# Performance work log

Hardware: AMD Instinct MI355X
Metric: run time of the kernel (lower is better)

## Reference

```python
import jax, jax.numpy as jnp
import numpy as np

E = 1024
H = 16
D = E // H  # head_dim = 64


def setup_inputs() -> dict:
    key = jax.random.key(0)
    k_x, k_w1, k_b1, k_w2, k_b2 = jax.random.split(key, 5)
    s = 1.0 / np.sqrt(E)
    return {
        "x": jax.random.normal(k_x, (2, 2048, E), dtype=jnp.float32),
        "qkv_w": jax.random.uniform(k_w1, (3 * E, E), jnp.float32, -s, s),
        "qkv_b": jax.random.uniform(k_b1, (3 * E,), jnp.float32, -s, s),
        "out_w": jax.random.uniform(k_w2, (E, E), jnp.float32, -s, s),
        "out_b": jax.random.uniform(k_b2, (E,), jnp.float32, -s, s),
    }


def reference(x, qkv_w, qkv_b, out_w, out_b):
    B, T, _ = x.shape
    # qkv projection (torch Linear: x @ W.T + b)
    qkv = x @ qkv_w.T + qkv_b  # [B, T, 3E]
    q, k, v = jnp.split(qkv, 3, axis=-1)
    # [B, T, E] -> [B, H, T, D]
    def to_heads(t):
        return t.reshape(B, T, H, D).transpose(0, 2, 1, 3)
    q, k, v = to_heads(q), to_heads(k), to_heads(v)
    scale = 1.0 / np.sqrt(D).astype(np.float32)
    scores = jnp.einsum("bhqd,bhkd->bhqk", q, k) * scale  # [B, H, T, T]
    attn = jax.nn.softmax(scores, axis=-1)
    # dropout is identity in eval mode
    out = jnp.einsum("bhqk,bhkd->bhqd", attn, v)  # [B, H, T, D]
    out = out.transpose(0, 2, 1, 3).reshape(B, T, E)
    return out @ out_w.T + out_b
```

## Files before the change

### kernel.cpp

```cpp
#include <hip/hip_runtime.h>

#define TT 2048
#define BB 2
#define EE 1024
#define HH 16
#define DD 64
#define E3 3072
#define NTOK 4096

typedef unsigned short u16;
typedef _Float16 __attribute__((ext_vector_type(8))) half8;
typedef __fp16 __attribute__((ext_vector_type(2))) fp16x2;
typedef __attribute__((ext_vector_type(4))) float f32x4;

__device__ __forceinline__ unsigned f2h(float f) {
    union { _Float16 h; u16 u; } v; v.h = (_Float16)f; return (unsigned)v.u;
}
__device__ __forceinline__ unsigned pkh(float a, float b) {
    union { fp16x2 h; unsigned u; } v;
    v.h = __builtin_amdgcn_cvt_pkrtz(a, b);
    return v.u;
}

__device__ __forceinline__ void async_ld16(const u16* g, const u16* l) {
    auto gp = reinterpret_cast<const __attribute__((address_space(1))) unsigned*>(
        reinterpret_cast<uintptr_t>(g));
    auto lp = reinterpret_cast<__attribute__((address_space(3))) unsigned*>(
        reinterpret_cast<uintptr_t>(l));
    __builtin_amdgcn_global_load_lds(gp, lp, 16, 0, 0);
}

__global__ __launch_bounds__(256) void split3(
    const float* __restrict__ x, const float* __restrict__ w1,
    const float* __restrict__ w2,
    u16* __restrict__ xh, u16* __restrict__ w1h, u16* __restrict__ w2h)
{
    const int N1 = (NTOK * EE) / 4;
    const int N2 = N1 + (E3 * EE) / 4;
    int i = blockIdx.x * 256 + threadIdx.x;
    const float* src; u16* dst; int j;
    if (i < N1)      { src = x;  dst = xh;  j = i; }
    else if (i < N2) { src = w1; dst = w1h; j = i - N1; }
    else             { src = w2; dst = w2h; j = i - N2; }
    float4 v = ((const float4*)src)[j];
    *(uint2*)&dst[(size_t)j * 4] = make_uint2(
        f2h(v.x) | (f2h(v.y) << 16), f2h(v.z) | (f2h(v.w) << 16));
}

template <int WMT, bool QSCALE, bool F16OUT>
__global__ __launch_bounds__(256, 3) void gemm_f16(
    const u16* __restrict__ Ag, const u16* __restrict__ Wg,
    const float* __restrict__ bias, void* __restrict__ Cout,
    u16* __restrict__ vtp, int M, int N)
{
    constexpr int BM = WMT * 32;
    constexpr int APASS = BM / 32;
    __shared__ u16 sAB[(BM + 128) * 64];
    u16* sA = sAB;
    u16* sB = sAB + BM * 64;

    const int tid  = threadIdx.x;
    const int lane = tid & 63;
    const int wave = tid >> 6;
    const int quad = lane >> 4;
    const int l16  = lane & 15;
    const int wm = wave >> 1, wn = wave & 1;
    const int m0 = blockIdx.y * BM;
    const int n0 = blockIdx.x * 128;

    const int srow = tid >> 3;
    const int schk = tid & 7;

    const u16* ag[APASS]; int aldw[APASS];
#pragma unroll
    for (int p = 0; p < APASS; ++p) {
        int row = p * 32 + srow;
        ag[p] = Ag + (size_t)(m0 + row) * EE + ((schk ^ (row & 7)) << 3);
        aldw[p] = (p * 256 + wave * 64) * 8;
    }
    const u16* bg[4]; int bldw[4];
#pragma unroll
    for (int p = 0; p < 4; ++p) {
        int row = p * 32 + srow;
        bg[p] = Wg + (size_t)(n0 + row) * EE + ((schk ^ (row & 7)) << 3);
        bldw[p] = (p * 256 + wave * 64) * 8;
    }

    f32x4 acc[WMT][4];
#pragma unroll
    for (int mt = 0; mt < WMT; ++mt)
#pragma unroll
        for (int nt = 0; nt < 4; ++nt) acc[mt][nt] = (f32x4){0.f, 0.f, 0.f, 0.f};

    for (int k0 = 0; k0 < EE; k0 += 64) {
        __syncthreads();
#pragma unroll
        for (int p = 0; p < APASS; ++p) async_ld16(ag[p] + k0, sA + aldw[p]);
#pragma unroll
        for (int p = 0; p < 4; ++p)    async_ld16(bg[p] + k0, sB + bldw[p]);
        __syncthreads();

        half8 fa[WMT][2], fb[4][2];
#pragma unroll
        for (int mt = 0; mt < WMT; ++mt) {
            int r = wm * (WMT * 16) + mt * 16 + l16;
#pragma unroll
            for (int ks = 0; ks < 2; ++ks)
                fa[mt][ks] = *(const half8*)&sA[r * 64 + (((ks * 4 + quad) ^ (r & 7)) << 3)];
        }
#pragma unroll
        for (int nt = 0; nt < 4; ++nt) {
            int r = wn * 64 + nt * 16 + l16;
#pragma unroll
            for (int ks = 0; ks < 2; ++ks)
                fb[nt][ks] = *(const half8*)&sB[r * 64 + (((ks * 4 + quad) ^ (r & 7)) << 3)];
        }
#pragma unroll
        for (int ks = 0; ks < 2; ++ks)
#pragma unroll
            for (int mt = 0; mt < WMT; ++mt)
#pragma unroll
                for (int nt = 0; nt < 4; ++nt)
                    acc[mt][nt] = __builtin_amdgcn_mfma_f32_16x16x32_f16(
                        fa[mt][ks], fb[nt][ks], acc[mt][nt], 0, 0, 0);
    }

    const float scale = (QSCALE && n0 < EE) ? 0.18033688011112042f : 1.0f;
    float bv[4];
#pragma unroll
    for (int nt = 0; nt < 4; ++nt) bv[nt] = bias[n0 + wn * 64 + nt * 16 + l16];

    if constexpr (F16OUT) {
        if (vtp != nullptr && n0 >= 2 * EE) {
            __syncthreads();
            u16* tile = sAB;
#pragma unroll
            for (int mt = 0; mt < WMT; ++mt)
#pragma unroll
                for (int nt = 0; nt < 4; ++nt) {
                    int c  = wn * 64 + nt * 16 + l16;
                    int ub = (wm * 16 + mt * 4 + quad) ^ ((c & 7) << 1);
                    *(uint2*)&tile[c * 128 + ub * 4] = make_uint2(
                        f2h(acc[mt][nt][0] + bv[nt]) | (f2h(acc[mt][nt][1] + bv[nt]) << 16),
                        f2h(acc[mt][nt][2] + bv[nt]) | (f2h(acc[mt][nt][3] + bv[nt]) << 16));
                }
            __syncthreads();
            const int c    = tid >> 1;
            const int hf   = tid & 1;
            const int hd   = ((n0 - 2 * EE) >> 6) + (c >> 6);
            const int d    = c & 63;
            const int bq   = m0 >> 11;
            u16* dst = vtp + ((size_t)(bq * HH + hd) * DD + d) * TT
                           + (m0 & (TT - 1)) + hf * 64;
#pragma unroll
            for (int j = 0; j < 8; ++j) {
                int u = (hf * 16 + j * 2) ^ ((c & 7) << 1);
                *(uint4*)(dst + j * 8) = *(const uint4*)&tile[c * 128 + u * 4];
            }
            return;
        }
    }

#pragma unroll
    for (int mt = 0; mt < WMT; ++mt)
#pragma unroll
        for (int nt = 0; nt < 4; ++nt)
#pragma unroll
            for (int r = 0; r < 4; ++r) {
                int rg = m0 + wm * (WMT * 16) + mt * 16 + quad * 4 + r;
                int cg = n0 + wn * 64 + nt * 16 + l16;
                float v = (acc[mt][nt][r] + bv[nt]) * scale;
                if (F16OUT) ((u16*)Cout)[(size_t)rg * N + cg] = (u16)f2h(v);
                else        ((float*)Cout)[(size_t)rg * N + cg] = v;
            }
}

__global__ __launch_bounds__(256, 4) void attn_mfma(
    const u16* __restrict__ qkv, const u16* __restrict__ vt,
    u16* __restrict__ obuf)
{
    __shared__ u16 KB[2][64][64];
    __shared__ u16 VB[2][64][64];
    __shared__ u16 PB[4][16][64];

    const int tid  = threadIdx.x;
    const int wave = tid >> 6;
    const int lane = tid & 63;
    const int quad = lane >> 4;
    const int l16  = lane & 15;

    const int q0 = blockIdx.x * 64;
    const int hh = blockIdx.y;
    const int b  = blockIdx.z;

    const int srow = tid >> 3;
    const int schk = tid & 7;
    const int ldsw = wave * 512;

    half8 qb[2];
    {
        int row = q0 + wave * 16 + l16;
        const u16* qg = qkv + (size_t)(b * TT + row) * E3 + hh * DD;
        qb[0] = *(const half8*)(qg + quad * 8);
        qb[1] = *(const half8*)(qg + 32 + quad * 8);
    }

#pragma unroll
    for (int p = 0; p < 2; ++p) {
        int row = p * 32 + srow;
        int sw8 = (schk ^ (row & 7)) << 3;
        async_ld16(qkv + (size_t)(b * TT + row) * E3 + EE + hh * DD + sw8,
                   &KB[0][0][0] + p * 2048 + ldsw);
        async_ld16(vt + ((size_t)(b * HH + hh) * DD + row) * TT + sw8,
                   &VB[0][0][0] + p * 2048 + ldsw);
    }
    __syncthreads();

    const f32x4 Z = {0.f, 0.f, 0.f, 0.f};
    float l_i = 0.f;
    f32x4 o[4];
#pragma unroll
    for (int dt = 0; dt < 4; ++dt) o[dt] = (f32x4){0.f, 0.f, 0.f, 0.f};

    const int px = (l16 & 7) << 1;
    u16* prow = &PB[wave][l16][0];

    int cur = 0;
    for (int kt = 0; kt < TT; kt += 64, cur ^= 1) {
        const int ktn = (kt + 64) & (TT - 1);
#pragma unroll
        for (int p = 0; p < 2; ++p) {
            int row = p * 32 + srow;
            int sw8 = (schk ^ (row & 7)) << 3;
            async_ld16(qkv + (size_t)(b * TT + ktn + row) * E3 + EE + hh * DD + sw8,
                       &KB[cur ^ 1][0][0] + p * 2048 + ldsw);
            async_ld16(vt + ((size_t)(b * HH + hh) * DD + row) * TT + ktn + sw8,
                       &VB[cur ^ 1][0][0] + p * 2048 + ldsw);
        }

#pragma unroll
        for (int kg = 0; kg < 4; ++kg) {
            int r0 = kg * 16 + l16;
            half8 kf0 = *(const half8*)&KB[cur][r0][((quad)     ^ (r0 & 7)) << 3];
            half8 kf1 = *(const half8*)&KB[cur][r0][((4 + quad) ^ (r0 & 7)) << 3];
            f32x4 t = __builtin_amdgcn_mfma_f32_16x16x32_f16(kf0, qb[0], Z, 0, 0, 0);
            f32x4 s = __builtin_amdgcn_mfma_f32_16x16x32_f16(kf1, qb[1], t, 0, 0, 0);
            float p0 = __builtin_amdgcn_exp2f(s[0]);
            float p1 = __builtin_amdgcn_exp2f(s[1]);
            float p2 = __builtin_amdgcn_exp2f(s[2]);
            float p3 = __builtin_amdgcn_exp2f(s[3]);
            l_i += (p0 + p1) + (p2 + p3);
            int pu = (kg * 4 + quad) ^ px;
            *(uint2*)&prow[pu * 4] = make_uint2(pkh(p0, p1), pkh(p2, p3));
        }

#pragma unroll
        for (int kb = 0; kb < 2; ++kb) {
            half8 pf = *(const half8*)&prow[((kb * 8 + quad * 2) ^ px) << 2];
#pragma unroll
            for (int dt = 0; dt < 4; ++dt) {
                int vr = dt * 16 + l16;
                half8 vf = *(const half8*)&VB[cur][vr][((kb * 4 + quad) ^ (vr & 7)) << 3];
                o[dt] = __builtin_amdgcn_mfma_f32_16x16x32_f16(vf, pf, o[dt], 0, 0, 0);
            }
        }

        __syncthreads();
    }

    float inv;
    {
        float l = l_i;
        l += __shfl_xor(l, 16, 64);
        l += __shfl_xor(l, 32, 64);
        inv = 1.f / l;
    }
    {
        size_t base = (size_t)(b * TT + q0 + wave * 16 + l16) * EE + hh * DD;
#pragma unroll
        for (int dt = 0; dt < 4; ++dt) {
            unsigned h0 = f2h(o[dt][0] * inv), h1 = f2h(o[dt][1] * inv);
            unsigned h2 = f2h(o[dt][2] * inv), h3 = f2h(o[dt][3] * inv);
            *(uint2*)&obuf[base + dt * 16 + quad * 4] =
                make_uint2(h0 | (h1 << 16), h2 | (h3 << 16));
        }
    }
}

extern "C" void kernel_launch(void* const* d_in, const int* in_sizes, int n_in,
                              void* d_out, int out_size, void* d_ws, size_t ws_size,
                              hipStream_t stream)
{
    const float* x     = (const float*)d_in[0];
    const float* qkv_w = (const float*)d_in[1];
    const float* qkv_b = (const float*)d_in[2];
    const float* out_w = (const float*)d_in[3];
    const float* out_b = (const float*)d_in[4];
    float* out = (float*)d_out;

    const size_t NX  = (size_t)NTOK * EE;
    const size_t NW1 = (size_t)E3 * EE;
    const size_t NW2 = (size_t)EE * EE;
    const size_t NQ  = (size_t)NTOK * E3;

    u16* ws   = (u16*)d_ws;
    u16* x_h  = ws;
    u16* w1h  = ws + NX;
    u16* w2h  = w1h + NW1;
    u16* qkvb = w2h + NW2;
    u16* vtb  = qkvb + NQ;

    split3<<<dim3((unsigned)((NX + NW1 + NW2) / 4 / 256)), 256, 0, stream>>>(
        x, qkv_w, out_w, x_h, w1h, w2h);

    gemm_f16<4, true, true><<<dim3(E3 / 128, NTOK / 128), 256, 0, stream>>>(
        x_h, w1h, qkv_b, (void*)qkvb, vtb, NTOK, E3);

    attn_mfma<<<dim3(TT / 64, HH, BB), 256, 0, stream>>>(qkvb, vtb, x_h);

    gemm_f16<2, false, false><<<dim3(EE / 128, NTOK / 64), 256, 0, stream>>>(
        x_h, w2h, out_b, (void*)out, nullptr, NTOK, EE);
}
```

Baseline: 183.9 us.

## Restructure attention around 32x32 MFMA with register-resident probabilities

```diff
diff --git a/kernel.cpp b/kernel.cpp
--- a/kernel.cpp
+++ b/kernel.cpp
@@ -12,6 +12,7 @@
 typedef _Float16 __attribute__((ext_vector_type(8))) half8;
 typedef __fp16 __attribute__((ext_vector_type(2))) fp16x2;
 typedef __attribute__((ext_vector_type(4))) float f32x4;
+typedef __attribute__((ext_vector_type(16))) float f32x16;
 
 __device__ __forceinline__ unsigned f2h(float f) {
     union { _Float16 h; u16 u; } v; v.h = (_Float16)f; return (unsigned)v.u;
@@ -175,115 +176,125 @@
             }
 }
 
-__global__ __launch_bounds__(256, 4) void attn_mfma(
+__global__ __launch_bounds__(256, 2) void attn_mfma(
     const u16* __restrict__ qkv, const u16* __restrict__ vt,
     u16* __restrict__ obuf)
 {
-    __shared__ u16 KB[2][64][64];
-    __shared__ u16 VB[2][64][64];
-    __shared__ u16 PB[4][16][64];
+    __shared__ u16 VB[2][64][128];
 
     const int tid  = threadIdx.x;
     const int wave = tid >> 6;
     const int lane = tid & 63;
-    const int quad = lane >> 4;
-    const int l16  = lane & 15;
-
-    const int q0 = blockIdx.x * 64;
+    const int l31  = lane & 31;
+    const int h    = lane >> 5;
+
+    const int q0 = blockIdx.x * 128;
     const int hh = blockIdx.y;
     const int b  = blockIdx.z;
 
-    const int srow = tid >> 3;
-    const int schk = tid & 7;
-    const int ldsw = wave * 512;
-
-    half8 qb[2];
+    const int vrw  = lane >> 4;
+    const int vchk = lane & 15;
+
+    const u16* vbase = vt + (size_t)(b * HH + hh) * DD * TT;
+
+#pragma unroll
+    for (int p = 0; p < 4; ++p) {
+        int row = wave * 16 + p * 4 + vrw;
+        async_ld16(vbase + (size_t)row * TT + ((vchk ^ (row & 7)) << 3),
+                   &VB[0][0][0] + (wave * 16 + p * 4) * 128);
+    }
+
+    half8 qb[4];
     {
-        int row = q0 + wave * 16 + l16;
-        const u16* qg = qkv + (size_t)(b * TT + row) * E3 + hh * DD;
-        qb[0] = *(const half8*)(qg + quad * 8);
-        qb[1] = *(const half8*)(qg + 32 + quad * 8);
-    }
-
-#pragma unroll
-    for (int p = 0; p < 2; ++p) {
-        int row = p * 32 + srow;
-        int sw8 = (schk ^ (row & 7)) << 3;
-        async_ld16(qkv + (size_t)(b * TT + row) * E3 + EE + hh * DD + sw8,
-                   &KB[0][0][0] + p * 2048 + ldsw);
-        async_ld16(vt + ((size_t)(b * HH + hh) * DD + row) * TT + sw8,
-                   &VB[0][0][0] + p * 2048 + ldsw);
+        const u16* qg = qkv + (size_t)(b * TT + q0 + wave * 32 + l31) * E3 + hh * DD;
+#pragma unroll
+        for (int ks = 0; ks < 4; ++ks)
+            qb[ks] = *(const half8*)(qg + ks * 16 + h * 8);
     }
     __syncthreads();
 
-    const f32x4 Z = {0.f, 0.f, 0.f, 0.f};
+    f32x16 o[2];
+#pragma unroll
+    for (int dt = 0; dt < 2; ++dt)
+#pragma unroll
+        for (int j = 0; j < 16; ++j) o[dt][j] = 0.f;
     float l_i = 0.f;
-    f32x4 o[4];
-#pragma unroll
-    for (int dt = 0; dt < 4; ++dt) o[dt] = (f32x4){0.f, 0.f, 0.f, 0.f};
-
-    const int px = (l16 & 7) << 1;
-    u16* prow = &PB[wave][l16][0];
+
+    const f32x16 Z16 = {};
 
     int cur = 0;
-    for (int kt = 0; kt < TT; kt += 64, cur ^= 1) {
-        const int ktn = (kt + 64) & (TT - 1);
-#pragma unroll
-        for (int p = 0; p < 2; ++p) {
-            int row = p * 32 + srow;
-            int sw8 = (schk ^ (row & 7)) << 3;
-            async_ld16(qkv + (size_t)(b * TT + ktn + row) * E3 + EE + hh * DD + sw8,
-                       &KB[cur ^ 1][0][0] + p * 2048 + ldsw);
-            async_ld16(vt + ((size_t)(b * HH + hh) * DD + row) * TT + ktn + sw8,
-                       &VB[cur ^ 1][0][0] + p * 2048 + ldsw);
-        }
-
+    for (int kt = 0; kt < TT; kt += 128, cur ^= 1) {
+        const int ktn = (kt + 128) & (TT - 1);
+#pragma unroll
+        for (int p = 0; p < 4; ++p) {
+            int row = wave * 16 + p * 4 + vrw;
+            async_ld16(vbase + (size_t)row * TT + ktn + ((vchk ^ (row & 7)) << 3),
+                       &VB[cur ^ 1][0][0] + (wave * 16 + p * 4) * 128);
+        }
+
+        half8 kf[4][4];
 #pragma unroll
         for (int kg = 0; kg < 4; ++kg) {
-            int r0 = kg * 16 + l16;
-            half8 kf0 = *(const half8*)&KB[cur][r0][((quad)     ^ (r0 & 7)) << 3];
-            half8 kf1 = *(const half8*)&KB[cur][r0][((4 + quad) ^ (r0 & 7)) << 3];
-            f32x4 t = __builtin_amdgcn_mfma_f32_16x16x32_f16(kf0, qb[0], Z, 0, 0, 0);
-            f32x4 s = __builtin_amdgcn_mfma_f32_16x16x32_f16(kf1, qb[1], t, 0, 0, 0);
-            float p0 = __builtin_amdgcn_exp2f(s[0]);
-            float p1 = __builtin_amdgcn_exp2f(s[1]);
-            float p2 = __builtin_amdgcn_exp2f(s[2]);
-            float p3 = __builtin_amdgcn_exp2f(s[3]);
-            l_i += (p0 + p1) + (p2 + p3);
-            int pu = (kg * 4 + quad) ^ px;
-            *(uint2*)&prow[pu * 4] = make_uint2(pkh(p0, p1), pkh(p2, p3));
-        }
-
-#pragma unroll
-        for (int kb = 0; kb < 2; ++kb) {
-            half8 pf = *(const half8*)&prow[((kb * 8 + quad * 2) ^ px) << 2];
-#pragma unroll
-            for (int dt = 0; dt < 4; ++dt) {
-                int vr = dt * 16 + l16;
-                half8 vf = *(const half8*)&VB[cur][vr][((kb * 4 + quad) ^ (vr & 7)) << 3];
-                o[dt] = __builtin_amdgcn_mfma_f32_16x16x32_f16(vf, pf, o[dt], 0, 0, 0);
+            const u16* kgp = qkv + (size_t)(b * TT + kt + kg * 32 + l31) * E3
+                             + EE + hh * DD;
+#pragma unroll
+            for (int ks = 0; ks < 4; ++ks)
+                kf[kg][ks] = *(const half8*)(kgp + ks * 16 + h * 8);
+        }
+
+#pragma unroll
+        for (int kg = 0; kg < 4; ++kg) {
+            f32x16 c = Z16;
+#pragma unroll
+            for (int ks = 0; ks < 4; ++ks)
+                c = __builtin_amdgcn_mfma_f32_32x32x16_f16(kf[kg][ks], qb[ks], c, 0, 0, 0);
+
+            float p[16];
+#pragma unroll
+            for (int j = 0; j < 16; ++j) p[j] = __builtin_amdgcn_exp2f(c[j]);
+#pragma unroll
+            for (int j = 0; j < 16; ++j) l_i += p[j];
+
+#pragma unroll
+            for (int k2 = 0; k2 < 2; ++k2) {
+                const int e = k2 * 8;
+                unsigned x  = pkh(p[e + 0], p[e + 1]);
+                unsigned y  = pkh(p[e + 2], p[e + 3]);
+                unsigned xp = pkh(p[e + 4], p[e + 5]);
+                unsigned yp = pkh(p[e + 6], p[e + 7]);
+                asm("v_permlane32_swap_b32 %0, %1" : "+v"(x), "+v"(xp));
+                asm("v_permlane32_swap_b32 %0, %1" : "+v"(y), "+v"(yp));
+                union { unsigned u[4]; half8 v; } pu;
+                pu.u[0] = x; pu.u[1] = y; pu.u[2] = xp; pu.u[3] = yp;
+#pragma unroll
+                for (int dt = 0; dt < 2; ++dt) {
+                    int d = dt * 32 + l31;
+                    const half8 vf = *(const half8*)&VB[cur][d]
+                        [((kg * 4 + k2 * 2 + h) ^ (d & 7)) << 3];
+                    o[dt] = __builtin_amdgcn_mfma_f32_32x32x16_f16(vf, pu.v, o[dt], 0, 0, 0);
+                }
             }
         }
 
         __syncthreads();
     }
 
-    float inv;
+    l_i += __shfl_xor(l_i, 32, 64);
+    const float inv = 1.f / l_i;
     {
-        float l = l_i;
-        l += __shfl_xor(l, 16, 64);
-        l += __shfl_xor(l, 32, 64);
-        inv = 1.f / l;
-    }
-    {
-        size_t base = (size_t)(b * TT + q0 + wave * 16 + l16) * EE + hh * DD;
-#pragma unroll
-        for (int dt = 0; dt < 4; ++dt) {
-            unsigned h0 = f2h(o[dt][0] * inv), h1 = f2h(o[dt][1] * inv);
-            unsigned h2 = f2h(o[dt][2] * inv), h3 = f2h(o[dt][3] * inv);
-            *(uint2*)&obuf[base + dt * 16 + quad * 4] =
-                make_uint2(h0 | (h1 << 16), h2 | (h3 << 16));
-        }
+        size_t base = (size_t)(b * TT + q0 + wave * 32 + l31) * EE + hh * DD;
+#pragma unroll
+        for (int dt = 0; dt < 2; ++dt)
+#pragma unroll
+            for (int g = 0; g < 4; ++g) {
+                int d = dt * 32 + g * 8 + h * 4;
+                unsigned h0 = f2h(o[dt][g * 4 + 0] * inv);
+                unsigned h1 = f2h(o[dt][g * 4 + 1] * inv);
+                unsigned h2 = f2h(o[dt][g * 4 + 2] * inv);
+                unsigned h3 = f2h(o[dt][g * 4 + 3] * inv);
+                *(uint2*)&obuf[base + d] =
+                    make_uint2(h0 | (h1 << 16), h2 | (h3 << 16));
+            }
     }
 }
 
@@ -316,7 +327,7 @@
     gemm_f16<4, true, true><<<dim3(E3 / 128, NTOK / 128), 256, 0, stream>>>(
         x_h, w1h, qkv_b, (void*)qkvb, vtb, NTOK, E3);
 
-    attn_mfma<<<dim3(TT / 64, HH, BB), 256, 0, stream>>>(qkvb, vtb, x_h);
+    attn_mfma<<<dim3(TT / 128, HH, BB), 256, 0, stream>>>(qkvb, vtb, x_h);
 
     gemm_f16<2, false, false><<<dim3(EE / 128, NTOK / 64), 256, 0, stream>>>(
         x_h, w2h, out_b, (void*)out, nullptr, NTOK, EE);
```

Measured after the change: 218.7 us. +19.0%, slower.
